# Optimization experiments

Measured on AMD Instinct MI355X. Metric: run time of the kernel, lower is better.

The kernel has to match this reference:

```python
import jax, jax.numpy as jnp
import numpy as np

B, K, D, E, P = 256, 36, 2048, 1024, 5  # batch, regions, img_dim, embed_size, n_partial

def _xavier(key, fan_in, fan_out):
    r = np.sqrt(6.0) / np.sqrt(fan_in + fan_out)
    return jax.random.uniform(key, (fan_in, fan_out), minval=-r, maxval=r, dtype=jnp.float32)

def setup_inputs() -> dict:
    key = jax.random.key(0)
    ks = jax.random.split(key, 10)
    images = jax.random.normal(ks[0], (B, K, D), jnp.float32)
    bboxes = jax.random.uniform(ks[1], (B, K, 4), dtype=jnp.float32)
    img_range = jax.random.randint(ks[2], (B, K, K), 0, 2).astype(jnp.float32)
    z = lambda n: jnp.zeros((n,), jnp.float32)
    return dict(
        images=images, bboxes=bboxes, img_range=img_range,
        gate_w1=_xavier(ks[3], D + 5, D), gate_b1=z(D),
        gate_w2=_xavier(ks[4], D, 1), gate_b2=z(1),
        node_w1=_xavier(ks[5], D + 5, D), node_b1=z(D),
        node_w2=_xavier(ks[6], D, D), node_b2=z(D),
        map_w1=_xavier(ks[7], D, D), map_b1=z(D),
        map_w2=_xavier(ks[8], D, E), map_b2=z(E),
    )

def l2norm(x, eps=1e-8):
    return x / (jnp.sqrt(jnp.sum(x * x, axis=-1, keepdims=True)) + eps)

def reference(images, bboxes, img_range,
              gate_w1, gate_b1, gate_w2, gate_b2,
              node_w1, node_b1, node_w2, node_b2,
              map_w1, map_b1, map_w2, map_b2):
    # spatial info: bbox coords + area
    area = (bboxes[:, :, 2] - bboxes[:, :, 0]) * (bboxes[:, :, 3] - bboxes[:, :, 1])
    s_infos = jnp.concatenate([bboxes, area[:, :, None]], axis=2)  # (B,K,5)
    x = jnp.concatenate([images, s_infos * 0.1], axis=2)           # (B,K,D+5)

    gate = jnp.maximum(x @ gate_w1 + gate_b1, 0.0) @ gate_w2 + gate_b2  # (B,K,1)
    m = jax.nn.sigmoid(gate)[..., 0]                                     # (B,K)
    v = jnp.maximum(x @ node_w1 + node_b1, 0.0) @ node_w2 + node_b2      # (B,K,D)

    # top-P relation selection; fall back to self index when relation != 1
    effe_rels, topk_idx = jax.lax.top_k(img_range, P)                    # (B,K,P)
    idx_background = jnp.broadcast_to(jnp.arange(K)[None, :, None], (B, K, P))
    effe_ids = jnp.where(effe_rels == 1, topk_idx, idx_background)       # (B,K,P) int

    # per-batch gather of neighbor features/weights (no (B,K,K,D) repeat)
    v_gather = jax.vmap(lambda vb, ib: vb[ib])(v, effe_ids)              # (B,K,P,D)
    m_gather = jax.vmap(lambda mb, ib: mb[ib])(m, effe_ids)              # (B,K,P)

    out = jnp.einsum('bkp,bkpd->bkd', m_gather, v_gather)                # weighted sum
    out = l2norm(out)
    imgs = images + out
    img_emb = jnp.maximum(imgs @ map_w1 + map_b1, 0.0) @ map_w2 + map_b2  # (B,K,E)
    return l2norm(img_emb)
```

## Files before the change

kernel.cpp:

```cpp
#include <hip/hip_runtime.h>
#include <stdint.h>


typedef unsigned short ushort_t;
typedef unsigned int uint32;
typedef __bf16 bf16x8 __attribute__((ext_vector_type(8)));
typedef float f32x4 __attribute__((ext_vector_type(4)));

__device__ __forceinline__ ushort_t f2bf(float f) {
  uint32 u = __float_as_uint(f);
  u += 0x7fffu + ((u >> 16) & 1u);
  return (ushort_t)(u >> 16);
}
__device__ __forceinline__ float bflo(uint32 u) { return __uint_as_float(u << 16); }
__device__ __forceinline__ float bfhi(uint32 u) { return __uint_as_float(u & 0xffff0000u); }

__device__ __forceinline__ void gl_lds16(const void* g, void* l) {
  __builtin_amdgcn_global_load_lds(
      (__attribute__((address_space(1))) void*)(void*)g,
      (__attribute__((address_space(3))) void*)l, 16, 0, 0);
}

__device__ __forceinline__ float blk_sum(float v, float* sred) {
#pragma unroll
  for (int o = 32; o > 0; o >>= 1) v += __shfl_down(v, o, 64);
  const int w = threadIdx.x >> 6;
  if ((threadIdx.x & 63) == 0) sred[w] = v;
  __syncthreads();
  return sred[0] + sred[1] + sred[2] + sred[3];
}

__global__ __launch_bounds__(256) void transpose_all(
    const float* __restrict__ gw1, const float* __restrict__ nw1,
    const float* __restrict__ nw2, const float* __restrict__ mw1,
    const float* __restrict__ mw2,
    ushort_t* __restrict__ W1t, ushort_t* __restrict__ W2t,
    ushort_t* __restrict__ W3t, ushort_t* __restrict__ W4t) {
  __shared__ float tile[32][33];
  const float* src;
  ushort_t* dst;
  int RKsrc, RKdst, CN;
  switch (blockIdx.z) {
    case 0: src = gw1; dst = W1t;                        RKsrc = 2053; RKdst = 2080; CN = 2048; break;
    case 1: src = nw1; dst = W1t + (size_t)2048 * 2080;  RKsrc = 2053; RKdst = 2080; CN = 2048; break;
    case 2: src = nw2; dst = W2t;                        RKsrc = 2048; RKdst = 2048; CN = 2048; break;
    case 3: src = mw1; dst = W3t;                        RKsrc = 2048; RKdst = 2048; CN = 2048; break;
    default: src = mw2; dst = W4t;                       RKsrc = 2048; RKdst = 2048; CN = 1024; break;
  }
  const int bx = blockIdx.x, by = blockIdx.y;
  if (bx * 32 >= CN || by * 32 >= RKdst) return;
  const int c = bx * 32 + threadIdx.x;
#pragma unroll
  for (int t = 0; t < 4; ++t) {
    int r = by * 32 + threadIdx.y + t * 8;
    tile[threadIdx.y + t * 8][threadIdx.x] = (r < RKsrc) ? src[(size_t)r * CN + c] : 0.f;
  }
  __syncthreads();
  const int dc = by * 32 + threadIdx.x;
#pragma unroll
  for (int t = 0; t < 4; ++t) {
    int dr = bx * 32 + threadIdx.y + t * 8;
    dst[(size_t)dr * RKdst + dc] = f2bf(tile[threadIdx.x][threadIdx.y + t * 8]);
  }
}

__global__ __launch_bounds__(256) void build_A(const float* __restrict__ images,
                                               const float* __restrict__ bboxes,
                                               ushort_t* __restrict__ A) {
  const int row = blockIdx.x, tid = threadIdx.x;
  size_t i = (size_t)row * 2048 + tid * 8;
  float4 a = *(const float4*)(images + i);
  float4 b = *(const float4*)(images + i + 4);
  uint4 o;
  o.x = (uint32)f2bf(a.x) | ((uint32)f2bf(a.y) << 16);
  o.y = (uint32)f2bf(a.z) | ((uint32)f2bf(a.w) << 16);
  o.z = (uint32)f2bf(b.x) | ((uint32)f2bf(b.y) << 16);
  o.w = (uint32)f2bf(b.z) | ((uint32)f2bf(b.w) << 16);
  *(uint4*)(A + (size_t)row * 2080 + tid * 8) = o;
  if (tid < 4) {
    uint4 s = {0, 0, 0, 0};
    if (tid == 0) {
      const float* bb = bboxes + (size_t)row * 4;
      float s0 = bb[0], s1 = bb[1], s2 = bb[2], s3 = bb[3];
      float s4 = (s2 - s0) * (s3 - s1);
      s.x = (uint32)f2bf(0.1f * s0) | ((uint32)f2bf(0.1f * s1) << 16);
      s.y = (uint32)f2bf(0.1f * s2) | ((uint32)f2bf(0.1f * s3) << 16);
      s.z = (uint32)f2bf(0.1f * s4);
    }
    *(uint4*)(A + (size_t)row * 2080 + 2048 + tid * 8) = s;
  }
}

template <int MODE>
__global__ __launch_bounds__(256) void gemm_bt(
    const ushort_t* __restrict__ A, int lda,
    const ushort_t* __restrict__ Bt, int K,
    void* __restrict__ outp, int ldo,
    const float* __restrict__ bias, const float* __restrict__ bias2, int nsplit) {
  __shared__ ushort_t sA[128 * 32];
  __shared__ ushort_t sB[128 * 32];
  const int tid = threadIdx.x;
  const int w = tid >> 6, l = tid & 63;
  const int wm = (w >> 1) * 64, wn = (w & 1) * 64;
  const int lr = l >> 4, lc = l & 15;
  const int mBase = blockIdx.y * 128, cBase = blockIdx.x * 128;

  const int r0 = tid >> 2;
  const int c8 = (tid & 3) * 8;
  const ushort_t* gA = A + (size_t)(mBase + r0) * lda + c8;
  const ushort_t* gB = Bt + (size_t)(cBase + r0) * K + c8;
  const size_t sA64 = (size_t)64 * lda;
  const size_t sB64 = (size_t)64 * K;
  char* ldsA0 = (char*)sA + w * 1024;
  char* ldsA1 = (char*)sA + 4096 + w * 1024;
  char* ldsB0 = (char*)sB + w * 1024;
  char* ldsB1 = (char*)sB + 4096 + w * 1024;

  f32x4 acc[4][4] = {};

  for (int k0 = 0; k0 < K; k0 += 32) {
    gl_lds16(gA + k0, ldsA0);
    gl_lds16(gA + sA64 + k0, ldsA1);
    gl_lds16(gB + k0, ldsB0);
    gl_lds16(gB + sB64 + k0, ldsB1);
    __syncthreads();
    bf16x8 af[4], bfr[4];
#pragma unroll
    for (int i = 0; i < 4; ++i)
      af[i] = *(const bf16x8*)&sA[(wm + i * 16 + lc) * 32 + lr * 8];
#pragma unroll
    for (int j = 0; j < 4; ++j)
      bfr[j] = *(const bf16x8*)&sB[(wn + j * 16 + lc) * 32 + lr * 8];
#pragma unroll
    for (int i = 0; i < 4; ++i)
#pragma unroll
      for (int j = 0; j < 4; ++j)
        acc[i][j] = __builtin_amdgcn_mfma_f32_16x16x32_bf16(af[i], bfr[j], acc[i][j], 0, 0, 0);
    __syncthreads();
  }

  const float* bp = (cBase < nsplit) ? bias : bias2;
  const int cof = (cBase < nsplit) ? 0 : nsplit;
  float bcol[4];
#pragma unroll
  for (int j = 0; j < 4; ++j) bcol[j] = bp[cBase + wn + j * 16 + lc - cof];
#pragma unroll
  for (int i = 0; i < 4; ++i)
#pragma unroll
    for (int e = 0; e < 4; ++e) {
      size_t rg = mBase + wm + i * 16 + lr * 4 + e;
#pragma unroll
      for (int j = 0; j < 4; ++j) {
        float v = acc[i][j][e] + bcol[j];
        if (MODE == 0 && v < 0.f) v = 0.f;
        size_t oi = rg * ldo + (cBase + wn + j * 16 + lc);
        if (MODE == 2) ((float*)outp)[oi] = v;
        else ((ushort_t*)outp)[oi] = f2bf(v);
      }
    }
}

__global__ __launch_bounds__(256) void gate2_k(const ushort_t* __restrict__ hcat,
                                               const float* __restrict__ gw2,
                                               const float* __restrict__ gb2,
                                               float* __restrict__ msig) {
  __shared__ float sred[4];
  const int row = blockIdx.x;
  const int d0 = threadIdx.x * 8;
  uint4 u = *(const uint4*)(hcat + (size_t)row * 4096 + d0);
  float4 w0 = *(const float4*)(gw2 + d0);
  float4 w1 = *(const float4*)(gw2 + d0 + 4);
  float s = bflo(u.x) * w0.x + bfhi(u.x) * w0.y + bflo(u.y) * w0.z + bfhi(u.y) * w0.w +
            bflo(u.z) * w1.x + bfhi(u.z) * w1.y + bflo(u.w) * w1.z + bfhi(u.w) * w1.w;
  float tot = blk_sum(s, sred);
  if (threadIdx.x == 0) msig[row] = 1.f / (1.f + expf(-(tot + gb2[0])));
}

__global__ __launch_bounds__(256) void aggregate_k(const float* __restrict__ img_range,
                                                   const float* __restrict__ msig,
                                                   const ushort_t* __restrict__ vbf,
                                                   const float* __restrict__ images,
                                                   ushort_t* __restrict__ imgs_out) {
  __shared__ int s_id[5];
  __shared__ float s_w[5];
  __shared__ float sred[4];
  const int row = blockIdx.x;
  const int b = row / 36, k = row - b * 36;
  const int tid = threadIdx.x;
  if (tid < 64) {
    float val = (tid < 36) ? img_range[(size_t)row * 36 + tid] : 0.f;
    unsigned long long mask = __ballot(val == 1.0f);
    if (tid < 5) {
      unsigned long long mm = mask;
      for (int p = 0; p < tid; ++p) mm &= (mm - 1);
      int id = mm ? (int)__builtin_ctzll(mm) : k;
      s_id[tid] = id;
      s_w[tid] = msig[b * 36 + id];
    }
  }
  __syncthreads();
  const int d0 = tid * 8;
  float acc8[8] = {0, 0, 0, 0, 0, 0, 0, 0};
#pragma unroll
  for (int p = 0; p < 5; ++p) {
    uint4 u = *(const uint4*)(vbf + ((size_t)(b * 36 + s_id[p])) * 2048 + d0);
    float wg = s_w[p];
    acc8[0] += wg * bflo(u.x); acc8[1] += wg * bfhi(u.x);
    acc8[2] += wg * bflo(u.y); acc8[3] += wg * bfhi(u.y);
    acc8[4] += wg * bflo(u.z); acc8[5] += wg * bfhi(u.z);
    acc8[6] += wg * bflo(u.w); acc8[7] += wg * bfhi(u.w);
  }
  float ss = 0;
#pragma unroll
  for (int e = 0; e < 8; ++e) ss += acc8[e] * acc8[e];
  float tot = blk_sum(ss, sred);
  float inv = 1.f / (sqrtf(tot) + 1e-8f);
  const float* im = images + (size_t)row * 2048 + d0;
  float4 x0 = *(const float4*)im;
  float4 x1 = *(const float4*)(im + 4);
  float r[8] = {x0.x + acc8[0] * inv, x0.y + acc8[1] * inv, x0.z + acc8[2] * inv,
                x0.w + acc8[3] * inv, x1.x + acc8[4] * inv, x1.y + acc8[5] * inv,
                x1.z + acc8[6] * inv, x1.w + acc8[7] * inv};
  uint4 o;
  o.x = (uint32)f2bf(r[0]) | ((uint32)f2bf(r[1]) << 16);
  o.y = (uint32)f2bf(r[2]) | ((uint32)f2bf(r[3]) << 16);
  o.z = (uint32)f2bf(r[4]) | ((uint32)f2bf(r[5]) << 16);
  o.w = (uint32)f2bf(r[6]) | ((uint32)f2bf(r[7]) << 16);
  *(uint4*)(imgs_out + (size_t)row * 2048 + d0) = o;
}

__global__ __launch_bounds__(256) void l2norm_k(const float* __restrict__ emb,
                                                float* __restrict__ out) {
  __shared__ float sred[4];
  size_t base = (size_t)blockIdx.x * 1024 + threadIdx.x * 4;
  float4 x = *(const float4*)(emb + base);
  float tot = blk_sum(x.x * x.x + x.y * x.y + x.z * x.z + x.w * x.w, sred);
  float inv = 1.f / (sqrtf(tot) + 1e-8f);
  float4 o = {x.x * inv, x.y * inv, x.z * inv, x.w * inv};
  *(float4*)(out + base) = o;
}

extern "C" void kernel_launch(void* const* d_in, const int* in_sizes, int n_in,
                              void* d_out, int out_size, void* d_ws, size_t ws_size,
                              hipStream_t stream) {
  (void)in_sizes; (void)n_in; (void)out_size; (void)ws_size;
  const float* images    = (const float*)d_in[0];
  const float* bboxes    = (const float*)d_in[1];
  const float* img_range = (const float*)d_in[2];
  const float* gate_w1   = (const float*)d_in[3];
  const float* gate_b1   = (const float*)d_in[4];
  const float* gate_w2   = (const float*)d_in[5];
  const float* gate_b2   = (const float*)d_in[6];
  const float* node_w1   = (const float*)d_in[7];
  const float* node_b1   = (const float*)d_in[8];
  const float* node_w2   = (const float*)d_in[9];
  const float* node_b2   = (const float*)d_in[10];
  const float* map_w1    = (const float*)d_in[11];
  const float* map_b1    = (const float*)d_in[12];
  const float* map_w2    = (const float*)d_in[13];
  const float* map_b2    = (const float*)d_in[14];

  char* ws = (char*)d_ws;
  size_t off = 0;
  auto take = [&](size_t bytes) {
    char* p = ws + off;
    off += (bytes + 255) & ~(size_t)255;
    return p;
  };
  ushort_t* W1t  = (ushort_t*)take((size_t)4096 * 2080 * 2);
  ushort_t* W2t  = (ushort_t*)take((size_t)2048 * 2048 * 2);
  ushort_t* W3t  = (ushort_t*)take((size_t)2048 * 2048 * 2);
  ushort_t* W4t  = (ushort_t*)take((size_t)1024 * 2048 * 2);
  ushort_t* Abuf = (ushort_t*)take((size_t)9216 * 2080 * 2);
  ushort_t* Hcat = (ushort_t*)take((size_t)9216 * 4096 * 2);
  ushort_t* Vbuf = (ushort_t*)take((size_t)9216 * 2048 * 2);
  float*    Msig = (float*)take((size_t)9216 * 4);
  float*    Emb  = (float*)Vbuf;

  transpose_all<<<dim3(64, 65, 5), dim3(32, 8), 0, stream>>>(
      gate_w1, node_w1, node_w2, map_w1, map_w2, W1t, W2t, W3t, W4t);
  build_A<<<9216, 256, 0, stream>>>(images, bboxes, Abuf);

  gemm_bt<0><<<dim3(32, 72), 256, 0, stream>>>(Abuf, 2080, W1t, 2080, Hcat, 4096,
                                               gate_b1, node_b1, 2048);
  gate2_k<<<9216, 256, 0, stream>>>(Hcat, gate_w2, gate_b2, Msig);
  gemm_bt<1><<<dim3(16, 72), 256, 0, stream>>>(Hcat + 2048, 4096, W2t, 2048, Vbuf, 2048,
                                               node_b2, node_b2, 1 << 30);
  aggregate_k<<<9216, 256, 0, stream>>>(img_range, Msig, Vbuf, images, Abuf);
  gemm_bt<0><<<dim3(16, 72), 256, 0, stream>>>(Abuf, 2048, W3t, 2048, Hcat, 2048,
                                               map_b1, map_b1, 1 << 30);
  gemm_bt<2><<<dim3(8, 72), 256, 0, stream>>>(Hcat, 2048, W4t, 2048, Emb, 1024,
                                              map_b2, map_b2, 1 << 30);
  l2norm_k<<<9216, 256, 0, stream>>>(Emb, (float*)d_out);
}
```

Before: 744.8 us.

## Fuse gate second layer into GEMM epilogue, deepen K step, merge prep kernels

The gate's second linear layer is folded into the epilogue of a dedicated gate GEMM. Each block writes per-64-column partial dot products, and aggregate_k reduces them and applies the sigmoid, so the gate hidden layer is never stored and gate2_k is dropped. The GEMM core now loads 64 K-elements per barrier pair, with the padded K rising from 2080 to 2112 to keep that a multiple of 64. The weight transpose and the A-matrix build are merged into one launch. In exchange, the first GEMM becomes two launches, and the padding adds a little extra work and memory traffic.

Measured after the change: 727.4 us. -2.3%, faster.

```diff
diff --git a/kernel.cpp b/kernel.cpp
--- a/kernel.cpp
+++ b/kernel.cpp
@@ -30,19 +30,48 @@
   return sred[0] + sred[1] + sred[2] + sred[3];
 }
 
-__global__ __launch_bounds__(256) void transpose_all(
+__global__ __launch_bounds__(256) void prep_k(
     const float* __restrict__ gw1, const float* __restrict__ nw1,
     const float* __restrict__ nw2, const float* __restrict__ mw1,
     const float* __restrict__ mw2,
+    const float* __restrict__ images, const float* __restrict__ bboxes,
     ushort_t* __restrict__ W1t, ushort_t* __restrict__ W2t,
-    ushort_t* __restrict__ W3t, ushort_t* __restrict__ W4t) {
+    ushort_t* __restrict__ W3t, ushort_t* __restrict__ W4t,
+    ushort_t* __restrict__ Abuf) {
   __shared__ float tile[32][33];
+  const int z = blockIdx.z;
+  if (z >= 5) {
+    const int tid = threadIdx.y * 32 + threadIdx.x;
+    const int row = (z - 5) * 4608 + blockIdx.y * 64 + blockIdx.x;
+    size_t i = (size_t)row * 2048 + tid * 8;
+    float4 a = *(const float4*)(images + i);
+    float4 b = *(const float4*)(images + i + 4);
+    uint4 o;
+    o.x = (uint32)f2bf(a.x) | ((uint32)f2bf(a.y) << 16);
+    o.y = (uint32)f2bf(a.z) | ((uint32)f2bf(a.w) << 16);
+    o.z = (uint32)f2bf(b.x) | ((uint32)f2bf(b.y) << 16);
+    o.w = (uint32)f2bf(b.z) | ((uint32)f2bf(b.w) << 16);
+    *(uint4*)(Abuf + (size_t)row * 2112 + tid * 8) = o;
+    if (tid < 8) {
+      uint4 s = {0, 0, 0, 0};
+      if (tid == 0) {
+        const float* bb = bboxes + (size_t)row * 4;
+        float s0 = bb[0], s1 = bb[1], s2 = bb[2], s3 = bb[3];
+        float s4 = (s2 - s0) * (s3 - s1);
+        s.x = (uint32)f2bf(0.1f * s0) | ((uint32)f2bf(0.1f * s1) << 16);
+        s.y = (uint32)f2bf(0.1f * s2) | ((uint32)f2bf(0.1f * s3) << 16);
+        s.z = (uint32)f2bf(0.1f * s4);
+      }
+      *(uint4*)(Abuf + (size_t)row * 2112 + 2048 + tid * 8) = s;
+    }
+    return;
+  }
   const float* src;
   ushort_t* dst;
   int RKsrc, RKdst, CN;
-  switch (blockIdx.z) {
-    case 0: src = gw1; dst = W1t;                        RKsrc = 2053; RKdst = 2080; CN = 2048; break;
-    case 1: src = nw1; dst = W1t + (size_t)2048 * 2080;  RKsrc = 2053; RKdst = 2080; CN = 2048; break;
+  switch (z) {
+    case 0: src = gw1; dst = W1t;                        RKsrc = 2053; RKdst = 2112; CN = 2048; break;
+    case 1: src = nw1; dst = W1t + (size_t)2048 * 2112;  RKsrc = 2053; RKdst = 2112; CN = 2048; break;
     case 2: src = nw2; dst = W2t;                        RKsrc = 2048; RKdst = 2048; CN = 2048; break;
     case 3: src = mw1; dst = W3t;                        RKsrc = 2048; RKdst = 2048; CN = 2048; break;
     default: src = mw2; dst = W4t;                       RKsrc = 2048; RKdst = 2048; CN = 1024; break;
@@ -64,86 +93,61 @@
   }
 }
 
-__global__ __launch_bounds__(256) void build_A(const float* __restrict__ images,
-                                               const float* __restrict__ bboxes,
-                                               ushort_t* __restrict__ A) {
-  const int row = blockIdx.x, tid = threadIdx.x;
-  size_t i = (size_t)row * 2048 + tid * 8;
-  float4 a = *(const float4*)(images + i);
-  float4 b = *(const float4*)(images + i + 4);
-  uint4 o;
-  o.x = (uint32)f2bf(a.x) | ((uint32)f2bf(a.y) << 16);
-  o.y = (uint32)f2bf(a.z) | ((uint32)f2bf(a.w) << 16);
-  o.z = (uint32)f2bf(b.x) | ((uint32)f2bf(b.y) << 16);
-  o.w = (uint32)f2bf(b.z) | ((uint32)f2bf(b.w) << 16);
-  *(uint4*)(A + (size_t)row * 2080 + tid * 8) = o;
-  if (tid < 4) {
-    uint4 s = {0, 0, 0, 0};
-    if (tid == 0) {
-      const float* bb = bboxes + (size_t)row * 4;
-      float s0 = bb[0], s1 = bb[1], s2 = bb[2], s3 = bb[3];
-      float s4 = (s2 - s0) * (s3 - s1);
-      s.x = (uint32)f2bf(0.1f * s0) | ((uint32)f2bf(0.1f * s1) << 16);
-      s.y = (uint32)f2bf(0.1f * s2) | ((uint32)f2bf(0.1f * s3) << 16);
-      s.z = (uint32)f2bf(0.1f * s4);
-    }
-    *(uint4*)(A + (size_t)row * 2080 + 2048 + tid * 8) = s;
-  }
-}
+#define GEMM_CORE(A, lda, Bt, K)                                                \
+  __shared__ ushort_t sA[2 * 128 * 32];                                         \
+  __shared__ ushort_t sB[2 * 128 * 32];                                         \
+  const int tid = threadIdx.x;                                                  \
+  const int w = tid >> 6, l = tid & 63;                                         \
+  const int wm = (w >> 1) * 64, wn = (w & 1) * 64;                              \
+  const int lr = l >> 4, lc = l & 15;                                           \
+  const int mBase = blockIdx.y * 128, cBase = blockIdx.x * 128;                 \
+  const int r0 = tid >> 2, c8 = (tid & 3) * 8;                                  \
+  const ushort_t* gA = (A) + (size_t)(mBase + r0) * (lda) + c8;                 \
+  const ushort_t* gB = (Bt) + (size_t)(cBase + r0) * (K) + c8;                  \
+  const size_t sA64 = (size_t)64 * (lda), sB64 = (size_t)64 * (K);              \
+  char* lA = (char*)sA + w * 1024;                                              \
+  char* lB = (char*)sB + w * 1024;                                              \
+  f32x4 acc[4][4] = {};                                                         \
+  for (int k0 = 0; k0 < (K); k0 += 64) {                                        \
+    gl_lds16(gA + k0, lA);                                                      \
+    gl_lds16(gA + sA64 + k0, lA + 4096);                                        \
+    gl_lds16(gA + k0 + 32, lA + 8192);                                          \
+    gl_lds16(gA + sA64 + k0 + 32, lA + 12288);                                  \
+    gl_lds16(gB + k0, lB);                                                      \
+    gl_lds16(gB + sB64 + k0, lB + 4096);                                        \
+    gl_lds16(gB + k0 + 32, lB + 8192);                                          \
+    gl_lds16(gB + sB64 + k0 + 32, lB + 12288);                                  \
+    __syncthreads();                                                            \
+    _Pragma("unroll")                                                           \
+    for (int kk = 0; kk < 2; ++kk) {                                            \
+      const ushort_t* pA = sA + kk * 4096;                                      \
+      const ushort_t* pB = sB + kk * 4096;                                      \
+      bf16x8 af[4], bfr[4];                                                     \
+      _Pragma("unroll")                                                         \
+      for (int i = 0; i < 4; ++i)                                               \
+        af[i] = *(const bf16x8*)&pA[(wm + i * 16 + lc) * 32 + lr * 8];          \
+      _Pragma("unroll")                                                         \
+      for (int j = 0; j < 4; ++j)                                               \
+        bfr[j] = *(const bf16x8*)&pB[(wn + j * 16 + lc) * 32 + lr * 8];         \
+      _Pragma("unroll")                                                         \
+      for (int i = 0; i < 4; ++i)                                               \
+        _Pragma("unroll")                                                       \
+        for (int j = 0; j < 4; ++j)                                             \
+          acc[i][j] = __builtin_amdgcn_mfma_f32_16x16x32_bf16(af[i], bfr[j],    \
+                                                              acc[i][j], 0, 0, 0); \
+    }                                                                           \
+    __syncthreads();                                                            \
+  }
 
 template <int MODE>
 __global__ __launch_bounds__(256) void gemm_bt(
     const ushort_t* __restrict__ A, int lda,
     const ushort_t* __restrict__ Bt, int K,
-    void* __restrict__ outp, int ldo,
-    const float* __restrict__ bias, const float* __restrict__ bias2, int nsplit) {
-  __shared__ ushort_t sA[128 * 32];
-  __shared__ ushort_t sB[128 * 32];
-  const int tid = threadIdx.x;
-  const int w = tid >> 6, l = tid & 63;
-  const int wm = (w >> 1) * 64, wn = (w & 1) * 64;
-  const int lr = l >> 4, lc = l & 15;
-  const int mBase = blockIdx.y * 128, cBase = blockIdx.x * 128;
-
-  const int r0 = tid >> 2;
-  const int c8 = (tid & 3) * 8;
-  const ushort_t* gA = A + (size_t)(mBase + r0) * lda + c8;
-  const ushort_t* gB = Bt + (size_t)(cBase + r0) * K + c8;
-  const size_t sA64 = (size_t)64 * lda;
-  const size_t sB64 = (size_t)64 * K;
-  char* ldsA0 = (char*)sA + w * 1024;
-  char* ldsA1 = (char*)sA + 4096 + w * 1024;
-  char* ldsB0 = (char*)sB + w * 1024;
-  char* ldsB1 = (char*)sB + 4096 + w * 1024;
-
-  f32x4 acc[4][4] = {};
-
-  for (int k0 = 0; k0 < K; k0 += 32) {
-    gl_lds16(gA + k0, ldsA0);
-    gl_lds16(gA + sA64 + k0, ldsA1);
-    gl_lds16(gB + k0, ldsB0);
-    gl_lds16(gB + sB64 + k0, ldsB1);
-    __syncthreads();
-    bf16x8 af[4], bfr[4];
-#pragma unroll
-    for (int i = 0; i < 4; ++i)
-      af[i] = *(const bf16x8*)&sA[(wm + i * 16 + lc) * 32 + lr * 8];
-#pragma unroll
-    for (int j = 0; j < 4; ++j)
-      bfr[j] = *(const bf16x8*)&sB[(wn + j * 16 + lc) * 32 + lr * 8];
-#pragma unroll
-    for (int i = 0; i < 4; ++i)
-#pragma unroll
-      for (int j = 0; j < 4; ++j)
-        acc[i][j] = __builtin_amdgcn_mfma_f32_16x16x32_bf16(af[i], bfr[j], acc[i][j], 0, 0, 0);
-    __syncthreads();
-  }
-
-  const float* bp = (cBase < nsplit) ? bias : bias2;
-  const int cof = (cBase < nsplit) ? 0 : nsplit;
+    void* __restrict__ outp, int ldo, const float* __restrict__ bias) {
+  GEMM_CORE(A, lda, Bt, K)
   float bcol[4];
 #pragma unroll
-  for (int j = 0; j < 4; ++j) bcol[j] = bp[cBase + wn + j * 16 + lc - cof];
+  for (int j = 0; j < 4; ++j) bcol[j] = bias[cBase + wn + j * 16 + lc];
 #pragma unroll
   for (int i = 0; i < 4; ++i)
 #pragma unroll
@@ -160,24 +164,52 @@
     }
 }
 
-__global__ __launch_bounds__(256) void gate2_k(const ushort_t* __restrict__ hcat,
-                                               const float* __restrict__ gw2,
-                                               const float* __restrict__ gb2,
-                                               float* __restrict__ msig) {
-  __shared__ float sred[4];
-  const int row = blockIdx.x;
-  const int d0 = threadIdx.x * 8;
-  uint4 u = *(const uint4*)(hcat + (size_t)row * 4096 + d0);
-  float4 w0 = *(const float4*)(gw2 + d0);
-  float4 w1 = *(const float4*)(gw2 + d0 + 4);
-  float s = bflo(u.x) * w0.x + bfhi(u.x) * w0.y + bflo(u.y) * w0.z + bfhi(u.y) * w0.w +
-            bflo(u.z) * w1.x + bfhi(u.z) * w1.y + bflo(u.w) * w1.z + bfhi(u.w) * w1.w;
-  float tot = blk_sum(s, sred);
-  if (threadIdx.x == 0) msig[row] = 1.f / (1.f + expf(-(tot + gb2[0])));
+__global__ __launch_bounds__(256) void gemm_gate(
+    const ushort_t* __restrict__ A, int lda,
+    const ushort_t* __restrict__ Bt, int K,
+    const float* __restrict__ bias, const float* __restrict__ gw2,
+    float* __restrict__ Gpart) {
+  GEMM_CORE(A, lda, Bt, K)
+  float bcol[4], g2c[4];
+#pragma unroll
+  for (int j = 0; j < 4; ++j) {
+    int c = cBase + wn + j * 16 + lc;
+    bcol[j] = bias[c];
+    g2c[j] = gw2[c];
+  }
+  float rsum[4][4];
+#pragma unroll
+  for (int i = 0; i < 4; ++i)
+#pragma unroll
+    for (int e = 0; e < 4; ++e) {
+      float ar = 0.f;
+#pragma unroll
+      for (int j = 0; j < 4; ++j) {
+        float v = acc[i][j][e] + bcol[j];
+        v = v > 0.f ? v : 0.f;
+        ar += v * g2c[j];
+      }
+      rsum[i][e] = ar;
+    }
+#pragma unroll
+  for (int m = 1; m < 16; m <<= 1)
+#pragma unroll
+    for (int i = 0; i < 4; ++i)
+#pragma unroll
+      for (int e = 0; e < 4; ++e) rsum[i][e] += __shfl_xor(rsum[i][e], m, 64);
+  if (lc == 0) {
+    const int colblk = (cBase + wn) >> 6;
+#pragma unroll
+    for (int i = 0; i < 4; ++i)
+#pragma unroll
+      for (int e = 0; e < 4; ++e)
+        Gpart[(size_t)(mBase + wm + i * 16 + lr * 4 + e) * 32 + colblk] = rsum[i][e];
+  }
 }
 
 __global__ __launch_bounds__(256) void aggregate_k(const float* __restrict__ img_range,
-                                                   const float* __restrict__ msig,
+                                                   const float* __restrict__ Gpart,
+                                                   const float* __restrict__ gb2,
                                                    const ushort_t* __restrict__ vbf,
                                                    const float* __restrict__ images,
                                                    ushort_t* __restrict__ imgs_out) {
@@ -190,12 +222,21 @@
   if (tid < 64) {
     float val = (tid < 36) ? img_range[(size_t)row * 36 + tid] : 0.f;
     unsigned long long mask = __ballot(val == 1.0f);
+    int myid = k;
     if (tid < 5) {
       unsigned long long mm = mask;
       for (int p = 0; p < tid; ++p) mm &= (mm - 1);
-      int id = mm ? (int)__builtin_ctzll(mm) : k;
-      s_id[tid] = id;
-      s_w[tid] = msig[b * 36 + id];
+      myid = mm ? (int)__builtin_ctzll(mm) : k;
+      s_id[tid] = myid;
+    }
+    const float bb = gb2[0];
+#pragma unroll
+    for (int p = 0; p < 5; ++p) {
+      int idp = __shfl(myid, p, 64);
+      float v = (tid < 32) ? Gpart[(size_t)(b * 36 + idp) * 32 + tid] : 0.f;
+#pragma unroll
+      for (int o = 16; o > 0; o >>= 1) v += __shfl_down(v, o, 64);
+      if (tid == 0) s_w[p] = 1.f / (1.f + expf(-(v + bb)));
     }
   }
   __syncthreads();
@@ -267,29 +308,27 @@
     off += (bytes + 255) & ~(size_t)255;
     return p;
   };
-  ushort_t* W1t  = (ushort_t*)take((size_t)4096 * 2080 * 2);
+  ushort_t* W1t  = (ushort_t*)take((size_t)4096 * 2112 * 2);
   ushort_t* W2t  = (ushort_t*)take((size_t)2048 * 2048 * 2);
   ushort_t* W3t  = (ushort_t*)take((size_t)2048 * 2048 * 2);
   ushort_t* W4t  = (ushort_t*)take((size_t)1024 * 2048 * 2);
-  ushort_t* Abuf = (ushort_t*)take((size_t)9216 * 2080 * 2);
-  ushort_t* Hcat = (ushort_t*)take((size_t)9216 * 4096 * 2);
+  ushort_t* Abuf = (ushort_t*)take((size_t)9216 * 2112 * 2);
+  ushort_t* Hn   = (ushort_t*)take((size_t)9216 * 2048 * 2);
   ushort_t* Vbuf = (ushort_t*)take((size_t)9216 * 2048 * 2);
-  float*    Msig = (float*)take((size_t)9216 * 4);
+  float*    Gpart = (float*)take((size_t)9216 * 32 * 4);
   float*    Emb  = (float*)Vbuf;
 
-  transpose_all<<<dim3(64, 65, 5), dim3(32, 8), 0, stream>>>(
-      gate_w1, node_w1, node_w2, map_w1, map_w2, W1t, W2t, W3t, W4t);
-  build_A<<<9216, 256, 0, stream>>>(images, bboxes, Abuf);
-
-  gemm_bt<0><<<dim3(32, 72), 256, 0, stream>>>(Abuf, 2080, W1t, 2080, Hcat, 4096,
-                                               gate_b1, node_b1, 2048);
-  gate2_k<<<9216, 256, 0, stream>>>(Hcat, gate_w2, gate_b2, Msig);
-  gemm_bt<1><<<dim3(16, 72), 256, 0, stream>>>(Hcat + 2048, 4096, W2t, 2048, Vbuf, 2048,
-                                               node_b2, node_b2, 1 << 30);
-  aggregate_k<<<9216, 256, 0, stream>>>(img_range, Msig, Vbuf, images, Abuf);
-  gemm_bt<0><<<dim3(16, 72), 256, 0, stream>>>(Abuf, 2048, W3t, 2048, Hcat, 2048,
-                                               map_b1, map_b1, 1 << 30);
-  gemm_bt<2><<<dim3(8, 72), 256, 0, stream>>>(Hcat, 2048, W4t, 2048, Emb, 1024,
-                                              map_b2, map_b2, 1 << 30);
+  prep_k<<<dim3(64, 72, 7), dim3(32, 8), 0, stream>>>(
+      gate_w1, node_w1, node_w2, map_w1, map_w2, images, bboxes,
+      W1t, W2t, W3t, W4t, Abuf);
+
+  gemm_bt<0><<<dim3(16, 72), 256, 0, stream>>>(Abuf, 2112, W1t + (size_t)2048 * 2112,
+                                               2112, Hn, 2048, node_b1);
+  gemm_gate<<<dim3(16, 72), 256, 0, stream>>>(Abuf, 2112, W1t, 2112,
+                                              gate_b1, gate_w2, Gpart);
+  gemm_bt<1><<<dim3(16, 72), 256, 0, stream>>>(Hn, 2048, W2t, 2048, Vbuf, 2048, node_b2);
+  aggregate_k<<<9216, 256, 0, stream>>>(img_range, Gpart, gate_b2, Vbuf, images, Abuf);
+  gemm_bt<0><<<dim3(16, 72), 256, 0, stream>>>(Abuf, 2048, W3t, 2048, Hn, 2048, map_b1);
+  gemm_bt<2><<<dim3(8, 72), 256, 0, stream>>>(Hn, 2048, W4t, 2048, Emb, 1024, map_b2);
   l2norm_k<<<9216, 256, 0, stream>>>(Emb, (float*)d_out);
 }
```
